# Optimization experiments

Measured on AMD Instinct MI355X. Metric: run time of the kernel, lower is better.

The kernel has to match this reference:

```python
import jax, jax.numpy as jnp
import numpy as np

B, T, E, V = 128, 24, 512, 30000
H2 = 2 * 512  # LSTMCell hidden size = 2*hidden_size per original code
IN = 2 * E    # token embedding concat image feature


def setup_inputs() -> dict:
    key = jax.random.key(0)
    ks = jax.random.split(key, 9)
    s = lambda fan: 1.0 / np.sqrt(fan)
    return {
        "features": jax.random.normal(ks[0], (B, E), jnp.float32),
        "captions": jax.random.randint(ks[1], (B, T), 0, V),
        "pad_idx": 0,
        "emb": jax.random.normal(ks[2], (V, E), jnp.float32),
        "W_ih": jax.random.uniform(ks[3], (4 * H2, IN), jnp.float32, -s(H2), s(H2)),
        "W_hh": jax.random.uniform(ks[4], (4 * H2, H2), jnp.float32, -s(H2), s(H2)),
        "b_ih": jax.random.uniform(ks[5], (4 * H2,), jnp.float32, -s(H2), s(H2)),
        "b_hh": jax.random.uniform(ks[6], (4 * H2,), jnp.float32, -s(H2), s(H2)),
        "W_out": jax.random.uniform(ks[7], (V, H2), jnp.float32, -s(H2), s(H2)),
        "b_out": jax.random.uniform(ks[8], (V,), jnp.float32, -s(H2), s(H2)),
    }


def reference(features, captions, pad_idx, emb, W_ih, W_hh, b_ih, b_hh, W_out, b_out):
    b = captions.shape[0]
    tok = emb[captions]                                   # [B,T,E]
    pad = jnp.broadcast_to(emb[pad_idx][None, None, :], (b, 1, E))
    seq = jnp.concatenate([pad, tok], axis=1)             # [B,T+1,E]
    feat = jnp.broadcast_to(features[:, None, :], (b, seq.shape[1], features.shape[1]))
    x = jnp.concatenate([seq, feat], axis=2)              # [B,T+1,2E]

    # precompute input-side gate projections for all timesteps (batched GEMM)
    xg = jnp.einsum('bti,gi->btg', x, W_ih) + b_ih + b_hh  # [B,T+1,4*H2]

    def step(carry, xg_t):
        h, c = carry
        g = xg_t + h @ W_hh.T                             # [B,4*H2]
        i, f, gg, o = jnp.split(g, 4, axis=-1)            # torch gate order i,f,g,o
        i, f, o = jax.nn.sigmoid(i), jax.nn.sigmoid(f), jax.nn.sigmoid(o)
        c = f * c + i * jnp.tanh(gg)
        h = o * jnp.tanh(c)
        return (h, c), h

    h0 = jnp.zeros((b, H2), x.dtype)
    c0 = jnp.zeros((b, H2), x.dtype)
    _, hs = jax.lax.scan(step, (h0, c0), jnp.swapaxes(xg, 0, 1))  # [T+1,B,H2]
    hs = jnp.swapaxes(hs, 0, 1)                           # [B,T+1,H2]

    logits = jnp.einsum('bth,vh->btv', hs, W_out) + b_out  # [B,T+1,V]
    predicted = jnp.transpose(logits[:, :-1, :], (0, 2, 1))  # [B,V,T]
    return predicted
```

## Files before the change

### kernel.cpp

```cpp
#include <hip/hip_runtime.h>
#include <hip/hip_bf16.h>
#include <math.h>

typedef unsigned short ushort_t;
typedef unsigned long long u64;
typedef __bf16 bf16x8 __attribute__((ext_vector_type(8)));
typedef float f32x4 __attribute__((ext_vector_type(4)));

#define BB 128
#define TT 24
#define EE 512
#define VV 30000
#define HH 1024
#define GG 4096
#define MM (BB*TT)
#define MPAD 30208

static __device__ __forceinline__ ushort_t f2bf(float x) {
  __hip_bfloat16 h = __float2bfloat16(x);
  return __builtin_bit_cast(ushort_t, h);
}

static __device__ __forceinline__ void gld_lds16(const void* g, void* l) {
  __builtin_amdgcn_global_load_lds((const __attribute__((address_space(1))) void*)g,
                                   (__attribute__((address_space(3))) void*)l, 16, 0, 0);
}

__global__ void prep_k(const float* __restrict__ Wih, const float* __restrict__ Whh,
                       const float* __restrict__ Wout,
                       const float* __restrict__ bi, const float* __restrict__ bh,
                       ushort_t* __restrict__ Wih_b, ushort_t* __restrict__ Whh_b,
                       ushort_t* __restrict__ Wout_b, float* __restrict__ bs) {
  const int bid = blockIdx.x, tid = threadIdx.x;
  const float* s; ushort_t* d; int n4, i0, stride;
  if (bid < 2048) {
    s = Wout; d = Wout_b; n4 = VV * HH / 4; i0 = bid * 256 + tid; stride = 2048 * 256;
  } else if (bid < 2560) {
    s = Wih; d = Wih_b; n4 = GG * HH / 4; i0 = (bid - 2048) * 256 + tid; stride = 512 * 256;
  } else if (bid < 3072) {
    s = Whh; d = Whh_b; n4 = GG * HH / 4; i0 = (bid - 2560) * 256 + tid; stride = 512 * 256;
  } else {
    for (int i = tid; i < GG; i += 256) bs[i] = bi[i] + bh[i];
    return;
  }
  for (int i = i0; i < n4; i += stride) {
    float4 v = reinterpret_cast<const float4*>(s)[i];
    ushort4 o;
    o.x = f2bf(v.x); o.y = f2bf(v.y); o.z = f2bf(v.z); o.w = f2bf(v.w);
    reinterpret_cast<ushort4*>(d)[i] = o;
  }
}

__global__ void build_xa_k(const float* __restrict__ emb, const int* __restrict__ captions,
                           const int* __restrict__ pad_idx, const float* __restrict__ features,
                           ushort_t* __restrict__ xa) {
  int row = blockIdx.x;
  int t = row >> 7;
  int b = row & 127;
  int cap = (t == 0) ? pad_idx[0] : captions[b * TT + (t - 1)];
  const float* s0 = emb + (size_t)cap * EE;
  const float* s1 = features + (size_t)b * EE;
  ushort_t* d = xa + (size_t)row * (2 * EE);
  for (int e = threadIdx.x; e < EE; e += 256) {
    d[e] = f2bf(s0[e]);
    d[EE + e] = f2bf(s1[e]);
  }
}

__global__ void zero_bar_k(int* __restrict__ bar) {
  for (int i = threadIdx.x; i < 1024; i += 256)
    __hip_atomic_store(&bar[i], 0, __ATOMIC_RELAXED, __HIP_MEMORY_SCOPE_AGENT);
}

__global__ __launch_bounds__(256) void gemm_xg(
    const ushort_t* __restrict__ A,
    const ushort_t* __restrict__ Bm,
    const float* __restrict__ bias,
    float* __restrict__ out)
{
  constexpr int K = 1024;
  __shared__ __align__(16) ushort_t As[2][8192];
  __shared__ __align__(16) ushort_t Bs[2][8192];
  const int bid = blockIdx.x;
  const int g = (bid & 7) * 96 + (bid >> 3);
  const int m0 = (g / 24) * 128;
  const int n0 = (g % 24) * 128;
  const int tid = threadIdx.x, wid = tid >> 6, lane = tid & 63;
  const int wm = (wid >> 1) * 64, wn_ = (wid & 1) * 64;
  const int srow = lane >> 3;
  const int scolsw = ((lane & 7) ^ srow) * 8;
  const int rr = lane & 15, l4 = lane >> 4;
  const int swz = (rr & 7) << 4;
  const int col0 = (((l4 << 4) ^ swz) >> 1);
  const int col1 = (((64 | (l4 << 4)) ^ swz) >> 1);

  f32x4 acc[4][4] = {};

  auto stage = [&](int buf, int k0) {
    #pragma unroll
    for (int p = 0; p < 4; ++p) {
      int ch = p * 4 + wid;
      int row = ch * 8 + srow;
      gld_lds16(A + (size_t)(m0 + row) * K + k0 + scolsw, &As[buf][ch * 512]);
      gld_lds16(Bm + (size_t)(n0 + row) * K + k0 + scolsw, &Bs[buf][ch * 512]);
    }
  };

  stage(0, 0);
  int cur = 0;
  for (int tau = 0; tau < 16; ++tau) {
    if (tau < 15) {
      stage(cur ^ 1, (tau + 1) * 64);
      asm volatile("s_waitcnt vmcnt(8)" ::: "memory");
    } else {
      asm volatile("s_waitcnt vmcnt(0)" ::: "memory");
    }
    __builtin_amdgcn_s_barrier();
    const ushort_t* Ac = As[cur];
    const ushort_t* Bc = Bs[cur];
    #pragma unroll
    for (int kk = 0; kk < 2; ++kk) {
      const int ce = kk ? col1 : col0;
      bf16x8 af[4], bfv[4];
      #pragma unroll
      for (int i = 0; i < 4; ++i)
        af[i] = *reinterpret_cast<const bf16x8*>(Ac + (wm + i * 16 + rr) * 64 + ce);
      #pragma unroll
      for (int j = 0; j < 4; ++j)
        bfv[j] = *reinterpret_cast<const bf16x8*>(Bc + (wn_ + j * 16 + rr) * 64 + ce);
      #pragma unroll
      for (int i = 0; i < 4; ++i)
        #pragma unroll
        for (int j = 0; j < 4; ++j)
          acc[i][j] = __builtin_amdgcn_mfma_f32_16x16x32_bf16(af[i], bfv[j], acc[i][j], 0, 0, 0);
    }
    asm volatile("" ::: "memory");
    __builtin_amdgcn_s_barrier();
    cur ^= 1;
  }

  const int l16 = lane & 15;
  #pragma unroll
  for (int i = 0; i < 4; ++i) {
    #pragma unroll
    for (int r = 0; r < 4; ++r) {
      int gi = m0 + wm + i * 16 + l4 * 4 + r;
      float bv = bias[gi];
      #pragma unroll
      for (int j = 0; j < 4; ++j) {
        int col = n0 + wn_ + j * 16 + l16;
        out[((size_t)(col >> 7) * GG + gi) * BB + (col & 127)] = acc[i][j][r] + bv;
      }
    }
  }
}

__global__ __launch_bounds__(512) void gemm256_logits(
    const ushort_t* __restrict__ A,
    const ushort_t* __restrict__ Bm,
    const float* __restrict__ bias,
    float* __restrict__ out)
{
  constexpr int K = 1024, NT = 16;
  __shared__ __align__(16) ushort_t As[2][16384];
  __shared__ __align__(16) ushort_t Bs[2][16384];
  const int bid = blockIdx.x;
  const int g = (bid & 7) * 177 + (bid >> 3);
  const int m0 = (g / 12) * 256, n0 = (g % 12) * 256;
  const int tid = threadIdx.x, wid = tid >> 6, lane = tid & 63;
  const int wm2 = wid >> 2, wn4 = wid & 3;
  const int rr = lane & 15, l4 = lane >> 4;

  f32x4 acc[8][4] = {};

  auto stage = [&](int buf, int kt, int ct) {
    const int k0 = kt * 64;
    #pragma unroll
    for (int l = 0; l < 2; ++l) {
      int f = l * 512 + tid;
      int lr = f >> 3;
      int ecol = k0 + (((f & 7) ^ (lr & 7)) * 8);
      if (ct == 0 || ct == 3) {
        int cc = (ct == 3);
        int grow = (lr & 63) + ((lr >> 6) << 7) + cc * 64;
        gld_lds16(A + (size_t)(m0 + grow) * K + ecol,
                  &As[buf][cc * 8192 + (l * 512 + wid * 64) * 8]);
      } else {
        int cc = ct - 1;
        int grow = ((lr >> 5) << 6) + cc * 32 + (lr & 31);
        gld_lds16(Bm + (size_t)(n0 + grow) * K + ecol,
                  &Bs[buf][cc * 8192 + (l * 512 + wid * 64) * 8]);
      }
    }
  };
  auto rdA = [&](int buf, int mf, int kk) -> bf16x8 {
    int rl = wm2 * 64 + (mf & 3) * 16 + rr;
    return *reinterpret_cast<const bf16x8*>(
        &As[buf][(mf >> 2) * 8192 + rl * 64 + (((kk * 4 + l4) ^ (rr & 7)) * 8)]);
  };
  auto rdB = [&](int buf, int nf, int kk) -> bf16x8 {
    int rl = wn4 * 32 + (nf & 1) * 16 + rr;
    return *reinterpret_cast<const bf16x8*>(
        &Bs[buf][(nf >> 1) * 8192 + rl * 64 + (((kk * 4 + l4) ^ (rr & 7)) * 8)]);
  };

  #pragma unroll
  for (int hh = 0; hh < 4; ++hh) stage(0, 0, hh);
  asm volatile("s_waitcnt vmcnt(4)" ::: "memory");
  __builtin_amdgcn_s_barrier();

  bf16x8 aF[4][2], bF[2][2], bF2[2][2];
  int cur = 0;
  for (int g2 = 0; g2 < NT; ++g2) {
    const int buf = cur, bufn = cur ^ 1;
    const int ktn = (g2 + 1 < NT) ? g2 + 1 : g2;
    #pragma unroll
    for (int mf = 0; mf < 4; ++mf) { aF[mf][0] = rdA(buf, mf, 0); aF[mf][1] = rdA(buf, mf, 1); }
    #pragma unroll
    for (int nf = 0; nf < 2; ++nf) { bF[nf][0] = rdB(buf, nf, 0); bF[nf][1] = rdB(buf, nf, 1); }
    stage(bufn, ktn, 0);
    __builtin_amdgcn_s_barrier();
    asm volatile("s_waitcnt lgkmcnt(0)" ::: "memory");
    __builtin_amdgcn_sched_barrier(0);
    __builtin_amdgcn_s_setprio(1);
    #pragma unroll
    for (int mf = 0; mf < 4; ++mf)
      #pragma unroll
      for (int nf = 0; nf < 2; ++nf) {
        acc[mf][nf] = __builtin_amdgcn_mfma_f32_16x16x32_bf16(aF[mf][0], bF[nf][0], acc[mf][nf], 0, 0, 0);
        acc[mf][nf] = __builtin_amdgcn_mfma_f32_16x16x32_bf16(aF[mf][1], bF[nf][1], acc[mf][nf], 0, 0, 0);
      }
    __builtin_amdgcn_s_setprio(0);
    asm volatile("s_waitcnt vmcnt(4)" ::: "memory");
    __builtin_amdgcn_s_barrier();
    #pragma unroll
    for (int nf = 0; nf < 2; ++nf) { bF2[nf][0] = rdB(buf, 2 + nf, 0); bF2[nf][1] = rdB(buf, 2 + nf, 1); }
    stage(bufn, ktn, 1);
    __builtin_amdgcn_s_barrier();
    asm volatile("s_waitcnt lgkmcnt(0)" ::: "memory");
    __builtin_amdgcn_sched_barrier(0);
    __builtin_amdgcn_s_setprio(1);
    #pragma unroll
    for (int mf = 0; mf < 4; ++mf)
      #pragma unroll
      for (int nf = 0; nf < 2; ++nf) {
        acc[mf][2 + nf] = __builtin_amdgcn_mfma_f32_16x16x32_bf16(aF[mf][0], bF2[nf][0], acc[mf][2 + nf], 0, 0, 0);
        acc[mf][2 + nf] = __builtin_amdgcn_mfma_f32_16x16x32_bf16(aF[mf][1], bF2[nf][1], acc[mf][2 + nf], 0, 0, 0);
      }
    __builtin_amdgcn_s_setprio(0);
    asm volatile("s_waitcnt vmcnt(4)" ::: "memory");
    __builtin_amdgcn_s_barrier();
    #pragma unroll
    for (int mf = 0; mf < 4; ++mf) { aF[mf][0] = rdA(buf, 4 + mf, 0); aF[mf][1] = rdA(buf, 4 + mf, 1); }
    stage(bufn, ktn, 2);
    __builtin_amdgcn_s_barrier();
    asm volatile("s_waitcnt lgkmcnt(0)" ::: "memory");
    __builtin_amdgcn_sched_barrier(0);
    __builtin_amdgcn_s_setprio(1);
    #pragma unroll
    for (int mf = 0; mf < 4; ++mf)
      #pragma unroll
      for (int nf = 0; nf < 2; ++nf) {
        acc[4 + mf][nf] = __builtin_amdgcn_mfma_f32_16x16x32_bf16(aF[mf][0], bF[nf][0], acc[4 + mf][nf], 0, 0, 0);
        acc[4 + mf][nf] = __builtin_amdgcn_mfma_f32_16x16x32_bf16(aF[mf][1], bF[nf][1], acc[4 + mf][nf], 0, 0, 0);
      }
    __builtin_amdgcn_s_setprio(0);
    __builtin_amdgcn_s_barrier();
    stage(bufn, ktn, 3);
    __builtin_amdgcn_s_barrier();
    __builtin_amdgcn_s_setprio(1);
    #pragma unroll
    for (int mf = 0; mf < 4; ++mf)
      #pragma unroll
      for (int nf = 0; nf < 2; ++nf) {
        acc[4 + mf][2 + nf] = __builtin_amdgcn_mfma_f32_16x16x32_bf16(aF[mf][0], bF2[nf][0], acc[4 + mf][2 + nf], 0, 0, 0);
        acc[4 + mf][2 + nf] = __builtin_amdgcn_mfma_f32_16x16x32_bf16(aF[mf][1], bF2[nf][1], acc[4 + mf][2 + nf], 0, 0, 0);
      }
    __builtin_amdgcn_s_setprio(0);
    asm volatile("s_waitcnt vmcnt(4)" ::: "memory");
    __builtin_amdgcn_s_barrier();
    cur ^= 1;
  }
  asm volatile("s_waitcnt vmcnt(0)" ::: "memory");

  const int vbase = m0 + wm2 * 128;
  const int nbase = n0 + wn4 * 64;
  size_t obase[4];
  #pragma unroll
  for (int nf = 0; nf < 4; ++nf) {
    int n = nbase + nf * 16 + rr;
    int bb = n / TT, tq = n - bb * TT;
    obase[nf] = (size_t)bb * ((size_t)VV * TT) + tq;
  }
  #pragma unroll
  for (int mf = 0; mf < 8; ++mf) {
    #pragma unroll
    for (int r = 0; r < 4; ++r) {
      int v = vbase + mf * 16 + l4 * 4 + r;
      if (v < VV) {
        float bv = bias[v];
        #pragma unroll
        for (int nf = 0; nf < 4; ++nf)
          out[obase[nf] + (size_t)v * TT] = acc[mf][nf][r] + bv;
      }
    }
  }
}

__global__ __launch_bounds__(512, 1) void lstm_seq_k(
    const ushort_t* __restrict__ Whh,
    const float* __restrict__ xgT,
    ushort_t* __restrict__ hs,
    int* __restrict__ bar)
{
  __shared__ f32x4 red[6][64][4];
  const int tid = threadIdx.x, wid = tid >> 6, lane = tid & 63;
  const int l16 = lane & 15, l4 = lane >> 4;
  const int bid = blockIdx.x;
  const int jblk = bid & 63, mblk = bid >> 6;
  const int j0 = jblk * 16, m0 = mblk * 32;
  const int ks = wid >> 1;
  const int msub = (wid & 1) * 16;
  int* flags = bar;
  const int fidx = (mblk << 6) | (ks << 4) | l16;

  bf16x8 Breg[4][8];
  #pragma unroll
  for (int g = 0; g < 4; ++g) {
    const ushort_t* bp = Whh + ((size_t)(g * 1024 + j0 + l16) << 10) + ks * 256 + l4 * 8;
    #pragma unroll
    for (int kc = 0; kc < 8; ++kc)
      Breg[g][kc] = *reinterpret_cast<const bf16x8*>(bp + kc * 32);
  }
  const int arow = m0 + msub + l16;
  float c_reg[4] = {0.f, 0.f, 0.f, 0.f};

  for (int t = 0; t < TT; ++t) {
    f32x4 acc[4] = {};
    f32x4 xv[4];
    if (ks == 0) {
      const float* xp = xgT + ((size_t)(t * GG + j0 + l16)) * BB + m0 + msub + l4 * 4;
      #pragma unroll
      for (int g = 0; g < 4; ++g)
        xv[g] = *reinterpret_cast<const f32x4*>(xp + (size_t)g * 1024 * BB);
    }
    if (t > 0) {
      const u64* Ab = reinterpret_cast<const u64*>(
          hs + (((size_t)arow * TT + (t - 1)) << 10) + ks * 256 + l4 * 8);
      bf16x8 afs[8];
      #pragma unroll
      for (int kc = 0; kc < 8; ++kc) {
        union { u64 q[2]; bf16x8 v; } u;
        u.q[0] = __hip_atomic_load(Ab + kc * 8,     __ATOMIC_RELAXED, __HIP_MEMORY_SCOPE_AGENT);
        u.q[1] = __hip_atomic_load(Ab + kc * 8 + 1, __ATOMIC_RELAXED, __HIP_MEMORY_SCOPE_AGENT);
        afs[kc] = u.v;
      }
      #pragma unroll
      for (int kc = 0; kc < 8; ++kc)
        #pragma unroll
        for (int g = 0; g < 4; ++g)
          acc[g] = __builtin_amdgcn_mfma_f32_16x16x32_bf16(afs[kc], Breg[g][kc], acc[g], 0, 0, 0);
    }
    if (ks != 0) {
      int slot = (ks - 1) * 2 + (wid & 1);
      #pragma unroll
      for (int g = 0; g < 4; ++g) red[slot][lane][g] = acc[g];
    }
    __syncthreads();
    if (ks == 0) {
      #pragma unroll
      for (int s = 0; s < 3; ++s)
        #pragma unroll
        for (int g = 0; g < 4; ++g)
          acc[g] += red[s * 2 + (wid & 1)][lane][g];
      #pragma unroll
      for (int r = 0; r < 4; ++r) {
        int b = m0 + msub + l4 * 4 + r;
        float gi = acc[0][r] + xv[0][r];
        float gf = acc[1][r] + xv[1][r];
        float gg = acc[2][r] + xv[2][r];
        float go = acc[3][r] + xv[3][r];
        gi = 1.f / (1.f + expf(-gi));
        gf = 1.f / (1.f + expf(-gf));
        go = 1.f / (1.f + expf(-go));
        float cn = gf * c_reg[r] + gi * tanhf(gg);
        c_reg[r] = cn;
        float hn = go * tanhf(cn);
        unsigned hv = (unsigned)f2bf(hn);
        unsigned pv = (unsigned)__shfl_xor((int)hv, 1);
        if (!(l16 & 1)) {
          unsigned pk = (hv & 0xffffu) | (pv << 16);
          __hip_atomic_store(
              reinterpret_cast<unsigned*>(hs + (((size_t)b * TT + t) << 10) + j0 + l16),
              pk, __ATOMIC_RELAXED, __HIP_MEMORY_SCOPE_AGENT);
        }
      }
    }
    if (t < TT - 1) {
      __syncthreads();
      if (tid == 0)
        __hip_atomic_store(&flags[bid], t + 1, __ATOMIC_RELAXED, __HIP_MEMORY_SCOPE_AGENT);
      for (;;) {
        int a = __hip_atomic_load(&flags[fidx], __ATOMIC_RELAXED, __HIP_MEMORY_SCOPE_AGENT);
        if (__all(a >= t + 1)) break;
        __builtin_amdgcn_s_sleep(1);
      }
    }
  }
}


extern "C" void kernel_launch(void* const* d_in, const int* in_sizes, int n_in,
                              void* d_out, int out_size, void* d_ws, size_t ws_size,
                              hipStream_t stream) {
  const float* features = (const float*)d_in[0];
  const int*   captions = (const int*)d_in[1];
  const int*   pad_idx  = (const int*)d_in[2];
  const float* emb      = (const float*)d_in[3];
  const float* W_ih     = (const float*)d_in[4];
  const float* W_hh     = (const float*)d_in[5];
  const float* b_ih     = (const float*)d_in[6];
  const float* b_hh     = (const float*)d_in[7];
  const float* W_out    = (const float*)d_in[8];
  const float* b_out    = (const float*)d_in[9];
  float* out = (float*)d_out;

  char* w = (char*)d_ws;
  auto carve = [&](size_t bytes) {
    char* p = w;
    w += (bytes + 255) & ~(size_t)255;
    return p;
  };
  ushort_t* Wih_b  = (ushort_t*)carve((size_t)GG * HH * 2);
  ushort_t* Whh_b  = (ushort_t*)carve((size_t)GG * HH * 2);
  ushort_t* Wout_b = (ushort_t*)carve((size_t)MPAD * HH * 2);
  ushort_t* xa     = (ushort_t*)carve((size_t)MM * HH * 2);
  float*    xgT    = (float*)carve((size_t)MM * GG * 4);
  ushort_t* hs     = (ushort_t*)carve((size_t)MM * HH * 2);
  float*    bsum   = (float*)carve((size_t)GG * 4);
  int*      bar    = (int*)carve(16384);

  prep_k<<<dim3(3073), 256, 0, stream>>>(W_ih, W_hh, W_out, b_ih, b_hh,
                                         Wih_b, Whh_b, Wout_b, bsum);
  build_xa_k<<<dim3(MM), 256, 0, stream>>>(emb, captions, pad_idx, features, xa);
  zero_bar_k<<<dim3(1), 256, 0, stream>>>(bar);

  gemm_xg<<<dim3(768), 256, 0, stream>>>(Wih_b, xa, bsum, xgT);

  lstm_seq_k<<<dim3(256), 512, 0, stream>>>(Whh_b, xgT, hs, bar);

  gemm256_logits<<<dim3(1416), 512, 0, stream>>>(Wout_b, hs, b_out, out);
}
```

Baseline: 571.7 us.

## Use hierarchical LSTM step barrier and reuse 256-tile GEMM for input projection

The per-timestep grid barrier in the LSTM kernel changes from every block polling 64 flags to a two-level scheme. One leader block per row group gathers its group's flags, then writes release flags spread on separate cache lines, and the other blocks each poll a single release flag. This is meant to cut global polling traffic and barrier latency across the 23 serial steps, at the cost of an extra hop. The input-gate GEMM also drops its dedicated 128x128 kernel for a templated 256x256 kernel (192 blocks), which trades parallelism for larger tiles.

After: 553.1 us. 1.03x faster.

```diff
diff --git a/kernel.cpp b/kernel.cpp
--- a/kernel.cpp
+++ b/kernel.cpp
@@ -68,94 +68,12 @@
 }
 
 __global__ void zero_bar_k(int* __restrict__ bar) {
-  for (int i = threadIdx.x; i < 1024; i += 256)
+  for (int i = threadIdx.x; i < 4096; i += 256)
     __hip_atomic_store(&bar[i], 0, __ATOMIC_RELAXED, __HIP_MEMORY_SCOPE_AGENT);
 }
 
-__global__ __launch_bounds__(256) void gemm_xg(
-    const ushort_t* __restrict__ A,
-    const ushort_t* __restrict__ Bm,
-    const float* __restrict__ bias,
-    float* __restrict__ out)
-{
-  constexpr int K = 1024;
-  __shared__ __align__(16) ushort_t As[2][8192];
-  __shared__ __align__(16) ushort_t Bs[2][8192];
-  const int bid = blockIdx.x;
-  const int g = (bid & 7) * 96 + (bid >> 3);
-  const int m0 = (g / 24) * 128;
-  const int n0 = (g % 24) * 128;
-  const int tid = threadIdx.x, wid = tid >> 6, lane = tid & 63;
-  const int wm = (wid >> 1) * 64, wn_ = (wid & 1) * 64;
-  const int srow = lane >> 3;
-  const int scolsw = ((lane & 7) ^ srow) * 8;
-  const int rr = lane & 15, l4 = lane >> 4;
-  const int swz = (rr & 7) << 4;
-  const int col0 = (((l4 << 4) ^ swz) >> 1);
-  const int col1 = (((64 | (l4 << 4)) ^ swz) >> 1);
-
-  f32x4 acc[4][4] = {};
-
-  auto stage = [&](int buf, int k0) {
-    #pragma unroll
-    for (int p = 0; p < 4; ++p) {
-      int ch = p * 4 + wid;
-      int row = ch * 8 + srow;
-      gld_lds16(A + (size_t)(m0 + row) * K + k0 + scolsw, &As[buf][ch * 512]);
-      gld_lds16(Bm + (size_t)(n0 + row) * K + k0 + scolsw, &Bs[buf][ch * 512]);
-    }
-  };
-
-  stage(0, 0);
-  int cur = 0;
-  for (int tau = 0; tau < 16; ++tau) {
-    if (tau < 15) {
-      stage(cur ^ 1, (tau + 1) * 64);
-      asm volatile("s_waitcnt vmcnt(8)" ::: "memory");
-    } else {
-      asm volatile("s_waitcnt vmcnt(0)" ::: "memory");
-    }
-    __builtin_amdgcn_s_barrier();
-    const ushort_t* Ac = As[cur];
-    const ushort_t* Bc = Bs[cur];
-    #pragma unroll
-    for (int kk = 0; kk < 2; ++kk) {
-      const int ce = kk ? col1 : col0;
-      bf16x8 af[4], bfv[4];
-      #pragma unroll
-      for (int i = 0; i < 4; ++i)
-        af[i] = *reinterpret_cast<const bf16x8*>(Ac + (wm + i * 16 + rr) * 64 + ce);
-      #pragma unroll
-      for (int j = 0; j < 4; ++j)
-        bfv[j] = *reinterpret_cast<const bf16x8*>(Bc + (wn_ + j * 16 + rr) * 64 + ce);
-      #pragma unroll
-      for (int i = 0; i < 4; ++i)
-        #pragma unroll
-        for (int j = 0; j < 4; ++j)
-          acc[i][j] = __builtin_amdgcn_mfma_f32_16x16x32_bf16(af[i], bfv[j], acc[i][j], 0, 0, 0);
-    }
-    asm volatile("" ::: "memory");
-    __builtin_amdgcn_s_barrier();
-    cur ^= 1;
-  }
-
-  const int l16 = lane & 15;
-  #pragma unroll
-  for (int i = 0; i < 4; ++i) {
-    #pragma unroll
-    for (int r = 0; r < 4; ++r) {
-      int gi = m0 + wm + i * 16 + l4 * 4 + r;
-      float bv = bias[gi];
-      #pragma unroll
-      for (int j = 0; j < 4; ++j) {
-        int col = n0 + wn_ + j * 16 + l16;
-        out[((size_t)(col >> 7) * GG + gi) * BB + (col & 127)] = acc[i][j][r] + bv;
-      }
-    }
-  }
-}
-
-__global__ __launch_bounds__(512) void gemm256_logits(
+template<int MODE>
+__global__ __launch_bounds__(512) void gemm256(
     const ushort_t* __restrict__ A,
     const ushort_t* __restrict__ Bm,
     const float* __restrict__ bias,
@@ -165,8 +83,14 @@
   __shared__ __align__(16) ushort_t As[2][16384];
   __shared__ __align__(16) ushort_t Bs[2][16384];
   const int bid = blockIdx.x;
-  const int g = (bid & 7) * 177 + (bid >> 3);
-  const int m0 = (g / 12) * 256, n0 = (g % 12) * 256;
+  int m0, n0;
+  if (MODE == 1) {
+    const int g = (bid & 7) * 177 + (bid >> 3);
+    m0 = (g / 12) * 256; n0 = (g % 12) * 256;
+  } else {
+    const int c = bid >> 3;
+    m0 = (c % 12) * 256; n0 = ((bid & 7) * 2 + c / 12) * 256;
+  }
   const int tid = threadIdx.x, wid = tid >> 6, lane = tid & 63;
   const int wm2 = wid >> 2, wn4 = wid & 3;
   const int rr = lane & 15, l4 = lane >> 4;
@@ -285,23 +209,39 @@
 
   const int vbase = m0 + wm2 * 128;
   const int nbase = n0 + wn4 * 64;
-  size_t obase[4];
-  #pragma unroll
-  for (int nf = 0; nf < 4; ++nf) {
-    int n = nbase + nf * 16 + rr;
-    int bb = n / TT, tq = n - bb * TT;
-    obase[nf] = (size_t)bb * ((size_t)VV * TT) + tq;
-  }
-  #pragma unroll
-  for (int mf = 0; mf < 8; ++mf) {
-    #pragma unroll
-    for (int r = 0; r < 4; ++r) {
-      int v = vbase + mf * 16 + l4 * 4 + r;
-      if (v < VV) {
-        float bv = bias[v];
+  if (MODE == 1) {
+    size_t obase[4];
+    #pragma unroll
+    for (int nf = 0; nf < 4; ++nf) {
+      int n = nbase + nf * 16 + rr;
+      int bb = n / TT, tq = n - bb * TT;
+      obase[nf] = (size_t)bb * ((size_t)VV * TT) + tq;
+    }
+    #pragma unroll
+    for (int mf = 0; mf < 8; ++mf) {
+      #pragma unroll
+      for (int r = 0; r < 4; ++r) {
+        int v = vbase + mf * 16 + l4 * 4 + r;
+        if (v < VV) {
+          float bv = bias[v];
+          #pragma unroll
+          for (int nf = 0; nf < 4; ++nf)
+            out[obase[nf] + (size_t)v * TT] = acc[mf][nf][r] + bv;
+        }
+      }
+    }
+  } else {
+    #pragma unroll
+    for (int mf = 0; mf < 8; ++mf) {
+      #pragma unroll
+      for (int nf = 0; nf < 4; ++nf) {
+        int n = nbase + nf * 16 + rr;
+        float bv = bias[n];
         #pragma unroll
-        for (int nf = 0; nf < 4; ++nf)
-          out[obase[nf] + (size_t)v * TT] = acc[mf][nf][r] + bv;
+        for (int r = 0; r < 4; ++r) {
+          int m = vbase + mf * 16 + l4 * 4 + r;
+          out[((size_t)(m >> 7) * GG + n) * BB + (m & 127)] = acc[mf][nf][r] + bv;
+        }
       }
     }
   }
@@ -322,7 +262,7 @@
   const int ks = wid >> 1;
   const int msub = (wid & 1) * 16;
   int* flags = bar;
-  const int fidx = (mblk << 6) | (ks << 4) | l16;
+  int* rel = bar + 256;
 
   bf16x8 Breg[4][8];
   #pragma unroll
@@ -398,13 +338,26 @@
     }
     if (t < TT - 1) {
       __syncthreads();
-      if (tid == 0)
-        __hip_atomic_store(&flags[bid], t + 1, __ATOMIC_RELAXED, __HIP_MEMORY_SCOPE_AGENT);
-      for (;;) {
-        int a = __hip_atomic_load(&flags[fidx], __ATOMIC_RELAXED, __HIP_MEMORY_SCOPE_AGENT);
-        if (__all(a >= t + 1)) break;
-        __builtin_amdgcn_s_sleep(1);
-      }
+      if (jblk == 0) {
+        if (wid == 0) {
+          if (lane == 0)
+            __hip_atomic_store(&flags[bid], t + 1, __ATOMIC_RELAXED, __HIP_MEMORY_SCOPE_AGENT);
+          for (;;) {
+            int a = __hip_atomic_load(&flags[(mblk << 6) | lane], __ATOMIC_RELAXED, __HIP_MEMORY_SCOPE_AGENT);
+            if (__all(a >= t + 1)) break;
+            __builtin_amdgcn_s_sleep(1);
+          }
+          if (lane < 8)
+            __hip_atomic_store(&rel[(mblk * 8 + lane) * 64], t + 1, __ATOMIC_RELAXED, __HIP_MEMORY_SCOPE_AGENT);
+        }
+      } else {
+        if (tid == 0) {
+          __hip_atomic_store(&flags[bid], t + 1, __ATOMIC_RELAXED, __HIP_MEMORY_SCOPE_AGENT);
+          while (__hip_atomic_load(&rel[(mblk * 8 + (jblk & 7)) * 64], __ATOMIC_RELAXED, __HIP_MEMORY_SCOPE_AGENT) < t + 1)
+            __builtin_amdgcn_s_sleep(1);
+        }
+      }
+      __syncthreads();
     }
   }
 }
@@ -445,9 +398,9 @@
   build_xa_k<<<dim3(MM), 256, 0, stream>>>(emb, captions, pad_idx, features, xa);
   zero_bar_k<<<dim3(1), 256, 0, stream>>>(bar);
 
-  gemm_xg<<<dim3(768), 256, 0, stream>>>(Wih_b, xa, bsum, xgT);
+  gemm256<0><<<dim3(192), 512, 0, stream>>>(xa, Wih_b, bsum, xgT);
 
   lstm_seq_k<<<dim3(256), 512, 0, stream>>>(Whh_b, xgT, hs, bar);
 
-  gemm256_logits<<<dim3(1416), 512, 0, stream>>>(Wout_b, hs, b_out, out);
-}
+  gemm256<1><<<dim3(1416), 512, 0, stream>>>(Wout_b, hs, b_out, out);
+}
```
